# Optimization experiments

Measured on AMD Instinct MI355X. Metric: run time of the kernel, lower is better.

Reference implementation:

```python
import jax, jax.numpy as jnp
import numpy as np

B, LT, D, H, DI = 8, 128, 512, 8, 2048
NMEM, LMEM = 1024, 64
DH = D // H
EPS = 1e-5
NEG = -1e9

def _ln(x, g, b):
    mu = x.mean(-1, keepdims=True)
    var = ((x - mu) ** 2).mean(-1, keepdims=True)
    return (x - mu) * jax.lax.rsqrt(var + EPS) * g + b

def _ffn(x, W1, b1, W2, b2):
    # PositionwiseFF with residual=True (dropout=0 / eval)
    return x + jax.nn.relu(x @ W1 + b1) @ W2 + b2

def setup_inputs():
    key = jax.random.key(0)
    ks = jax.random.split(key, 16)
    w = lambda i, shape: jax.random.normal(ks[i], shape, jnp.float32) * 0.02
    return {
        "dec_output": jax.random.normal(ks[0], (B, LT, D), jnp.float32),
        "mem_attn_out": jax.random.normal(ks[1], (B, LT, NMEM + 1), jnp.float32),
        "enc_out_mem": jax.random.normal(ks[2], (NMEM, LMEM, D), jnp.float32),
        "tgt_emb_mem": jax.random.normal(ks[3], (NMEM, LMEM, D), jnp.float32),
        "tgt_mask_mem": jax.random.randint(ks[4], (NMEM, LMEM), 0, 2, jnp.int32),
        "tgt_mask": jax.random.randint(ks[5], (B, LT), 0, 2, jnp.int32),
        "g0": jnp.ones((D,), jnp.float32), "be0": jnp.zeros((D,), jnp.float32),
        "g1": jnp.ones((D,), jnp.float32), "be1": jnp.zeros((D,), jnp.float32),
        "Wq": w(6, (D, D)), "bq": jnp.zeros((D,), jnp.float32),
        "Wk": w(7, (D, D)), "bk": jnp.zeros((D,), jnp.float32),
        "Wv": w(8, (D, D)), "bv": jnp.zeros((D,), jnp.float32),
        "Wo": w(9, (D, D)), "bo": jnp.zeros((D,), jnp.float32),
        "f1W1": w(10, (D, DI)), "f1b1": jnp.zeros((DI,), jnp.float32),
        "f1W2": w(11, (DI, D)), "f1b2": jnp.zeros((D,), jnp.float32),
        "f2W1": w(12, (D, DI)), "f2b1": jnp.zeros((DI,), jnp.float32),
        "f2W2": w(13, (DI, D)), "f2b2": jnp.zeros((D,), jnp.float32),
    }

def reference(dec_output, mem_attn_out, enc_out_mem, tgt_emb_mem, tgt_mask_mem, tgt_mask,
              g0, be0, g1, be1, Wq, bq, Wk, bk, Wv, bv, Wo, bo,
              f1W1, f1b1, f1W2, f1b2, f2W1, f2b1, f2W2, f2b2):
    x = _ln(dec_output, g0, be0)                       # [B,LT,D]
    N = B * LT
    samples = jnp.argmax(mem_attn_out, -1).reshape(N) - 1   # [-1, NMEM-1]
    valid = samples >= 0                               # [N]
    s = jnp.maximum(samples, 0)                        # clamp; masked later
    q = x.reshape(N, 1, D)
    # gather memory per selected query (torch compacts via unique; same math)
    k_in = enc_out_mem[s]                              # [N,LMEM,D]
    v_in = tgt_emb_mem[s]                              # [N,LMEM,D]
    kmask = tgt_mask_mem[s] != 0                       # True = valid key
    # multi-head attention, residual=True
    qh = (q @ Wq + bq).reshape(N, 1, H, DH).transpose(0, 2, 1, 3)     # [N,H,1,DH]
    kh = (k_in @ Wk + bk).reshape(N, LMEM, H, DH).transpose(0, 2, 1, 3)
    vh = (v_in @ Wv + bv).reshape(N, LMEM, H, DH).transpose(0, 2, 1, 3)
    scores = jnp.einsum('nhqd,nhkd->nhqk', qh, kh) / (DH ** 0.5)      # [N,H,1,LMEM]
    scores = jnp.where(kmask[:, None, None, :], scores, NEG)
    attn = jax.nn.softmax(scores, axis=-1)
    ctx = jnp.einsum('nhqk,nhkd->nhqd', attn, vh).transpose(0, 2, 1, 3).reshape(N, 1, D)
    st = q + ctx @ Wo + bo
    st = _ffn(st, f1W1, f1b1, f1W2, f1b2)
    st = _ln(st, g1, be1)
    # scatter back: positions with sample == -1 get zeros
    st = jnp.where(valid[:, None, None], st, 0.0)
    dec = x + st.reshape(B, LT, D)
    dec = _ffn(dec, f2W1, f2b1, f2W2, f2b2)
    return dec
```

## Files before the change

### kernel.cpp

```cpp
#include <hip/hip_runtime.h>
#include <math.h>

#define NQ   1024
#define DIM  512
#define NH   8
#define DHD  64
#define DFF  2048
#define LM   64

typedef __bf16 bf16x8 __attribute__((ext_vector_type(8)));
typedef float  f32x4  __attribute__((ext_vector_type(4)));

__device__ __forceinline__ unsigned short f2bf(float f) {
    unsigned u = __builtin_bit_cast(unsigned, f);
    return (unsigned short)((u + 0x7fffu + ((u >> 16) & 1u)) >> 16);
}
__device__ __forceinline__ float bflo(unsigned p) {
    return __builtin_bit_cast(float, p << 16);
}
__device__ __forceinline__ float bfhi(unsigned p) {
    return __builtin_bit_cast(float, p & 0xffff0000u);
}

__device__ __forceinline__ void gload16(const void* g, void* l) {
    __builtin_amdgcn_global_load_lds(
        (const __attribute__((address_space(1))) unsigned*)g,
        (__attribute__((address_space(3))) unsigned*)l, 16, 0, 0);
}

__device__ __forceinline__ float blk_sum(float v, volatile float* red) {
#pragma unroll
    for (int o = 32; o; o >>= 1) v += __shfl_down(v, o);
    __syncthreads();
    if ((threadIdx.x & 63) == 0) red[threadIdx.x >> 6] = v;
    __syncthreads();
    return red[0] + red[1] + red[2] + red[3];
}

struct PrepPtrs {
    const float* src[8];
    unsigned short* dst[8];
};
__global__ __launch_bounds__(256) void prep_ln0_k(
    PrepPtrs p,
    const float* __restrict__ dec_out, const float* __restrict__ attn_out,
    const float* __restrict__ g, const float* __restrict__ be,
    float* __restrict__ x, unsigned* __restrict__ xb, int* __restrict__ samples)
{
    __shared__ float tile[32][33];
    __shared__ float red[4];
    __shared__ float rv[4]; __shared__ int ri[4];
    const int bid = blockIdx.x;

    if (bid < 5120) {
        int m, lt;
        if (bid < 1024) { m = bid >> 8; lt = bid & 255; }
        else { m = 4 + ((bid - 1024) >> 10); lt = (bid - 1024) & 1023; }
        const int RS = (m < 4) ? 512 : ((m == 5 || m == 7) ? 2048 : 512);
        const int CS = (m < 4) ? 512 : ((m == 5 || m == 7) ? 512 : 2048);
        const int TC = CS >> 5;
        const int tr = lt / TC, tc = lt % TC;
        const float* s = p.src[m];
        unsigned short* d = p.dst[m];
        const int tx = threadIdx.x & 31, ty = threadIdx.x >> 5;
        if (m == 1) {
#pragma unroll
            for (int i = 0; i < 32; i += 8) {
                size_t idx = (size_t)(tr * 32 + ty + i) * CS + tc * 32 + tx;
                d[idx] = f2bf(s[idx]);
            }
        } else {
#pragma unroll
            for (int i = 0; i < 32; i += 8)
                tile[ty + i][tx] = s[(size_t)(tr * 32 + ty + i) * CS + tc * 32 + tx];
            __syncthreads();
#pragma unroll
            for (int i = 0; i < 32; i += 8)
                d[(size_t)(tc * 32 + ty + i) * RS + tr * 32 + tx] = f2bf(tile[tx][ty + i]);
        }
        return;
    }

    const int n = bid - 5120, t = threadIdx.x;
    float2 v = ((const float2*)(dec_out + (size_t)n * DIM))[t];
    float mu  = blk_sum(v.x + v.y, red) * (1.f / DIM);
    float dx = v.x - mu, dy = v.y - mu;
    float var = blk_sum(dx * dx + dy * dy, red) * (1.f / DIM);
    float rs = rsqrtf(var + 1e-5f);
    float2 gg = ((const float2*)g)[t], bb = ((const float2*)be)[t];
    float ox = dx * rs * gg.x + bb.x, oy = dy * rs * gg.y + bb.y;
    ((float2*)(x + (size_t)n * DIM))[t] = make_float2(ox, oy);
    xb[(size_t)n * 256 + t] = (unsigned)f2bf(ox) | ((unsigned)f2bf(oy) << 16);

    const float* ar = attn_out + (size_t)n * 1025;
    float bv = -INFINITY; int bi = 0x7fffffff;
    for (int i = t; i < 1025; i += 256) {
        float val = ar[i];
        if (val > bv || (val == bv && i < bi)) { bv = val; bi = i; }
    }
#pragma unroll
    for (int o = 32; o; o >>= 1) {
        float ov = __shfl_down(bv, o); int oi = __shfl_down(bi, o);
        if (ov > bv || (ov == bv && oi < bi)) { bv = ov; bi = oi; }
    }
    if ((t & 63) == 0) { rv[t >> 6] = bv; ri[t >> 6] = bi; }
    __syncthreads();
    if (t == 0) {
#pragma unroll
        for (int w = 1; w < 4; ++w)
            if (rv[w] > bv || (rv[w] == bv && ri[w] < bi)) { bv = rv[w]; bi = ri[w]; }
        samples[n] = bi - 1;
    }
}

template<bool RELU, bool BIAS, bool RES, bool WF32, bool WBF>
__global__ __launch_bounds__(256) void mfma_gemm(
    const unsigned short* __restrict__ A, const unsigned short* __restrict__ Bt,
    float* __restrict__ Cf, unsigned short* __restrict__ Cb,
    const float* __restrict__ bias, const float* __restrict__ res,
    int K, int lda, int ldb, int ldc,
    int sA, int sB, int sC, int sBias)
{
    __shared__ unsigned short Ab[2][64 * 64];
    __shared__ unsigned short Bb[2][64 * 64];
    const int t = threadIdx.x, lane = t & 63, wid = t >> 6;
    const int nx = gridDim.x;
    const int fid = blockIdx.y * nx + blockIdx.x;
    const int cpx = (nx * gridDim.y) >> 3;
    const int f2 = (fid & 7) * cpx + (fid >> 3);
    const int bn = (f2 % nx) * 64, bm = (f2 / nx) * 64, bz = blockIdx.z;
    const unsigned short* Abase = A + (size_t)bz * sA + (size_t)bm * lda;
    const unsigned short* Bbase = Bt + (size_t)bz * sB + (size_t)bn * ldb;

    const int r0 = wid * 16 + (lane >> 3);
    const int cbs = lane & 7;

#define STAGE_T(buf, base, ld, kt)                                              \
    {                                                                           \
        int r_ = r0;                                                            \
        gload16(base + (size_t)r_ * ld + (kt) * 64 + ((cbs ^ (r_ & 7)) << 3),   \
                &buf[(wid * 2 + 0) * 512]);                                     \
        r_ = r0 + 8;                                                            \
        gload16(base + (size_t)r_ * ld + (kt) * 64 + ((cbs ^ (r_ & 7)) << 3),   \
                &buf[(wid * 2 + 1) * 512]);                                     \
    }

    const int lr = lane & 15, lg = lane >> 4;
    const int wr = (wid >> 1) * 32, wc = (wid & 1) * 32;
    const int mA0 = wr + lr, mA1 = wr + 16 + lr;
    const int nB0 = wc + lr, nB1 = wc + 16 + lr;
    f32x4 acc[2][2] = {};

#define COMPUTE(b)                                                              \
    _Pragma("unroll")                                                           \
    for (int kk = 0; kk < 2; ++kk) {                                            \
        const int kb = kk * 4 + lg;                                             \
        bf16x8 a0 = *(const bf16x8*)&Ab[b][mA0 * 64 + ((kb ^ (mA0 & 7)) << 3)]; \
        bf16x8 a1 = *(const bf16x8*)&Ab[b][mA1 * 64 + ((kb ^ (mA1 & 7)) << 3)]; \
        bf16x8 b0 = *(const bf16x8*)&Bb[b][nB0 * 64 + ((kb ^ (nB0 & 7)) << 3)]; \
        bf16x8 b1 = *(const bf16x8*)&Bb[b][nB1 * 64 + ((kb ^ (nB1 & 7)) << 3)]; \
        acc[0][0] = __builtin_amdgcn_mfma_f32_16x16x32_bf16(a0, b0, acc[0][0], 0, 0, 0); \
        acc[0][1] = __builtin_amdgcn_mfma_f32_16x16x32_bf16(a0, b1, acc[0][1], 0, 0, 0); \
        acc[1][0] = __builtin_amdgcn_mfma_f32_16x16x32_bf16(a1, b0, acc[1][0], 0, 0, 0); \
        acc[1][1] = __builtin_amdgcn_mfma_f32_16x16x32_bf16(a1, b1, acc[1][1], 0, 0, 0); \
    }

    STAGE_T(Ab[0], Abase, lda, 0);
    STAGE_T(Bb[0], Bbase, ldb, 0);
    __syncthreads();
    const int NT = K >> 6;
    int cur = 0;
    for (int kt = 0; kt < NT; ++kt) {
        if (kt + 1 < NT) {
            STAGE_T(Ab[cur ^ 1], Abase, lda, kt + 1);
            STAGE_T(Bb[cur ^ 1], Bbase, ldb, kt + 1);
        }
        if (cur == 0) { COMPUTE(0); } else { COMPUTE(1); }
        __syncthreads();
        cur ^= 1;
    }

#pragma unroll
    for (int fm = 0; fm < 2; ++fm)
#pragma unroll
    for (int fn = 0; fn < 2; ++fn) {
        const int col = bn + wc + fn * 16 + lr;
        float bia = BIAS ? bias[bz * sBias + col] : 0.f;
#pragma unroll
        for (int r = 0; r < 4; ++r) {
            const int row = bm + wr + fm * 16 + lg * 4 + r;
            const size_t ci = (size_t)bz * sC + (size_t)row * ldc + col;
            float v = acc[fm][fn][r] + bia;
            if (RES) v += res[(size_t)row * ldc + col];
            if (RELU) v = fmaxf(v, 0.f);
            if (WF32) Cf[ci] = v;
            if (WBF)  Cb[ci] = f2bf(v);
        }
    }
#undef STAGE_T
#undef COMPUTE
}

__global__ __launch_bounds__(256) void attn_scores_k(
    const unsigned short* __restrict__ u_bf, const float* __restrict__ enc,
    const int* __restrict__ maskmem, const int* __restrict__ samples,
    unsigned short* __restrict__ p_half, float* __restrict__ msc)
{
    __shared__ float S_lds[2][32][8];
    const int n = blockIdx.x, kq = blockIdx.y, t = threadIdx.x;
    const int lane = t & 63, w = t >> 6;
    int s = samples[n]; if (s < 0) s = 0;

    const int keyloc = (w & 1) * 16 + (lane & 15);
    const int key = kq * 32 + keyloc;
    const int dh = w >> 1;
    const int lg = lane >> 4;
    const int h = lane & 15;
    const float4* kb = (const float4*)(enc + (size_t)s * (LM * DIM));
    const int base = key * 128 + dh * 64 + lg * 2;
    float4 pf[4][2];
#pragma unroll
    for (int ss = 0; ss < 4; ++ss) {
        pf[ss][0] = kb[base + ss * 8];
        pf[ss][1] = kb[base + ss * 8 + 1];
    }
    const unsigned short* ub = u_bf + (size_t)n * 4096 + (size_t)(h & 7) * 512 + dh * 256;
    f32x4 acc = {};
#pragma unroll
    for (int step = 0; step < 8; ++step) {
        float4 a0 = pf[step & 3][0], a1 = pf[step & 3][1];
        if (step + 4 < 8) {
            pf[step & 3][0] = kb[base + (step + 4) * 8];
            pf[step & 3][1] = kb[base + (step + 4) * 8 + 1];
        }
        bf16x8 af;
        af[0] = (__bf16)a0.x; af[1] = (__bf16)a0.y;
        af[2] = (__bf16)a0.z; af[3] = (__bf16)a0.w;
        af[4] = (__bf16)a1.x; af[5] = (__bf16)a1.y;
        af[6] = (__bf16)a1.z; af[7] = (__bf16)a1.w;
        bf16x8 bfr = *(const bf16x8*)&ub[(step * 4 + lg) * 8];
        acc = __builtin_amdgcn_mfma_f32_16x16x32_bf16(af, bfr, acc, 0, 0, 0);
    }
    if (h < 8) {
#pragma unroll
        for (int r = 0; r < 4; ++r)
            S_lds[dh][(w & 1) * 16 + lg * 4 + r][h] = acc[r];
    }
    __syncthreads();

    const int h2 = t >> 5, k2 = t & 31;
    float sc = (S_lds[0][k2][h2] + S_lds[1][k2][h2]) * 0.125f;
    const int mk = maskmem[(size_t)s * LM + kq * 32 + k2];
    sc = (mk != 0) ? sc : -1e9f;
    float m = sc;
#pragma unroll
    for (int o = 16; o; o >>= 1) m = fmaxf(m, __shfl_xor(m, o));
    float e = __expf(sc - m);
    float su = e;
#pragma unroll
    for (int o = 16; o; o >>= 1) su += __shfl_xor(su, o);
    p_half[((size_t)n * 2 + kq) * 256 + k2 * 8 + h2] = f2bf(e);
    if (k2 == 0)
        ((float2*)(msc + ((size_t)n * 2 + kq) * 16))[h2] = make_float2(m, su);
}

__global__ __launch_bounds__(256) void attn_pv_k(
    const unsigned short* __restrict__ p_half, const float* __restrict__ msc,
    const float* __restrict__ vemb, const int* __restrict__ samples,
    unsigned* __restrict__ a_bf)
{
    __shared__ uint4 P_lds[64];
    __shared__ float2 Red[3][8][64];
    __shared__ float Wh[2][8];
    const int dq = blockIdx.x, n = blockIdx.y, t = threadIdx.x;
    int s = samples[n]; if (s < 0) s = 0;

    if (t < 8) {
        float2 ms0 = ((const float2*)(msc + (size_t)n * 32))[t];
        float2 ms1 = ((const float2*)(msc + (size_t)n * 32 + 16))[t];
        float m = fmaxf(ms0.x, ms1.x);
        float w0 = __expf(ms0.x - m), w1 = __expf(ms1.x - m);
        float inv = 1.f / (ms0.y * w0 + ms1.y * w1);
        Wh[0][t] = w0 * inv; Wh[1][t] = w1 * inv;
    }
    __syncthreads();
    {
        const int k = t >> 2, hp = t & 3, kq = k >> 5;
        unsigned v = ((const unsigned*)p_half)[((size_t)n * 2 + kq) * 128 + (k & 31) * 4 + hp];
        float a = bflo(v) * Wh[kq][hp * 2];
        float b = bfhi(v) * Wh[kq][hp * 2 + 1];
        ((unsigned*)P_lds)[k * 4 + hp] = (unsigned)f2bf(a) | ((unsigned)f2bf(b) << 16);
    }
    __syncthreads();

    const int c = t & 63, kh = t >> 6;
    const float2* vb = (const float2*)(vemb + (size_t)s * (LM * DIM)) + dq * 64 + c;
    float2 acc8[8];
#pragma unroll
    for (int hh = 0; hh < 8; ++hh) acc8[hh] = make_float2(0.f, 0.f);
#pragma unroll 8
    for (int i = 0; i < 16; ++i) {
        const int k = kh * 16 + i;
        float2 v = vb[(size_t)k * 256];
        uint4 pr = P_lds[k];
        float p0 = bflo(pr.x), p1 = bfhi(pr.x);
        float p2 = bflo(pr.y), p3 = bfhi(pr.y);
        float p4 = bflo(pr.z), p5 = bfhi(pr.z);
        float p6 = bflo(pr.w), p7 = bfhi(pr.w);
        acc8[0].x = fmaf(p0, v.x, acc8[0].x); acc8[0].y = fmaf(p0, v.y, acc8[0].y);
        acc8[1].x = fmaf(p1, v.x, acc8[1].x); acc8[1].y = fmaf(p1, v.y, acc8[1].y);
        acc8[2].x = fmaf(p2, v.x, acc8[2].x); acc8[2].y = fmaf(p2, v.y, acc8[2].y);
        acc8[3].x = fmaf(p3, v.x, acc8[3].x); acc8[3].y = fmaf(p3, v.y, acc8[3].y);
        acc8[4].x = fmaf(p4, v.x, acc8[4].x); acc8[4].y = fmaf(p4, v.y, acc8[4].y);
        acc8[5].x = fmaf(p5, v.x, acc8[5].x); acc8[5].y = fmaf(p5, v.y, acc8[5].y);
        acc8[6].x = fmaf(p6, v.x, acc8[6].x); acc8[6].y = fmaf(p6, v.y, acc8[6].y);
        acc8[7].x = fmaf(p7, v.x, acc8[7].x); acc8[7].y = fmaf(p7, v.y, acc8[7].y);
    }
    if (kh > 0) {
#pragma unroll
        for (int hh = 0; hh < 8; ++hh) Red[kh - 1][hh][c] = acc8[hh];
    }
    __syncthreads();
    if (kh == 0) {
        unsigned* an = a_bf + (size_t)n * 2048 + dq * 64;
#pragma unroll
        for (int hh = 0; hh < 8; ++hh) {
            float2 r0 = Red[0][hh][c], r1 = Red[1][hh][c], r2 = Red[2][hh][c];
            float ox = acc8[hh].x + r0.x + r1.x + r2.x;
            float oy = acc8[hh].y + r0.y + r1.y + r2.y;
            an[hh * 256 + c] = (unsigned)f2bf(ox) | ((unsigned)f2bf(oy) << 16);
        }
    }
}

__global__ __launch_bounds__(256) void ln1_mask_add_k(
    const float* __restrict__ t1p, const float* __restrict__ st0,
    const float* __restrict__ b2, const float* __restrict__ g,
    const float* __restrict__ be, const int* __restrict__ samples,
    const float* __restrict__ x, float* __restrict__ dec, unsigned* __restrict__ decb)
{
    __shared__ float red[4];
    const int n = blockIdx.x, t = threadIdx.x;
    const size_t off = (size_t)n * DIM + t * 2;
    float2 p0 = *(const float2*)&t1p[off];
    float2 p1 = *(const float2*)&t1p[(size_t)NQ * DIM + off];
    float2 s0 = *(const float2*)&st0[off];
    float2 b2v = ((const float2*)b2)[t];
    float2 v = make_float2(p0.x + p1.x + s0.x + b2v.x, p0.y + p1.y + s0.y + b2v.y);
    float mu  = blk_sum(v.x + v.y, red) * (1.f / DIM);
    float dx = v.x - mu, dy = v.y - mu;
    float var = blk_sum(dx * dx + dy * dy, red) * (1.f / DIM);
    float rs = rsqrtf(var + 1e-5f);
    float2 gg = ((const float2*)g)[t], bb = ((const float2*)be)[t];
    float sx = dx * rs * gg.x + bb.x, sy = dy * rs * gg.y + bb.y;
    if (samples[n] < 0) { sx = 0.f; sy = 0.f; }
    float2 xx = *(const float2*)&x[off];
    float ox = xx.x + sx, oy = xx.y + sy;
    *(float2*)&dec[off] = make_float2(ox, oy);
    decb[(size_t)n * 256 + t] = (unsigned)f2bf(ox) | ((unsigned)f2bf(oy) << 16);
}

extern "C" void kernel_launch(void* const* d_in, const int* in_sizes, int n_in,
                              void* d_out, int out_size, void* d_ws, size_t ws_size,
                              hipStream_t stream)
{
    const float* dec_output = (const float*)d_in[0];
    const float* mem_attn   = (const float*)d_in[1];
    const float* enc_mem    = (const float*)d_in[2];
    const float* temb_mem   = (const float*)d_in[3];
    const int*   mask_mem   = (const int*)d_in[4];
    const float* g0  = (const float*)d_in[6];
    const float* be0 = (const float*)d_in[7];
    const float* g1  = (const float*)d_in[8];
    const float* be1 = (const float*)d_in[9];
    const float* Wq  = (const float*)d_in[10];
    const float* bq  = (const float*)d_in[11];
    const float* Wk  = (const float*)d_in[12];
    const float* Wv  = (const float*)d_in[14];
    const float* bv  = (const float*)d_in[15];
    const float* Wo  = (const float*)d_in[16];
    const float* bo  = (const float*)d_in[17];
    const float* f1W1 = (const float*)d_in[18];
    const float* f1b1 = (const float*)d_in[19];
    const float* f1W2 = (const float*)d_in[20];
    const float* f1b2 = (const float*)d_in[21];
    const float* f2W1 = (const float*)d_in[22];
    const float* f2b1 = (const float*)d_in[23];
    const float* f2W2 = (const float*)d_in[24];
    const float* f2b2 = (const float*)d_in[25];
    float* out = (float*)d_out;

    float* ws = (float*)d_ws;
    float*          x_f   = ws + 0;
    unsigned*       x_b   = (unsigned*)(ws + 524288);
    unsigned short* qh_b  = (unsigned short*)(ws + 786432);
    unsigned short* u_b   = (unsigned short*)(ws + 1048576);
    unsigned short* a_b   = (unsigned short*)(ws + 3145728);
    unsigned short* p_hlf = (unsigned short*)(ws + 5242880);
    float*          msc   = ws + 5505024;
    unsigned short* wqt   = (unsigned short*)(ws + 7340032);
    unsigned short* wkc   = (unsigned short*)(ws + 7471104);
    unsigned short* wvt   = (unsigned short*)(ws + 7602176);
    unsigned short* wot   = (unsigned short*)(ws + 7733248);
    unsigned short* f1w1t = (unsigned short*)(ws + 7864320);
    unsigned short* f1w2t = (unsigned short*)(ws + 8388608);
    unsigned short* f2w1t = (unsigned short*)(ws + 8912896);
    unsigned short* f2w2t = (unsigned short*)(ws + 9437184);
    int*            smp   = (int*)(ws + 9961472);
    float*          t1p_f = ws + 9962496;
    float*          st0_f = (float*)u_b + 0;
    unsigned short* st0_b = (unsigned short*)((float*)u_b + 524288);
    float*          dec_f = (float*)u_b + 655360;
    unsigned*       dec_b = (unsigned*)((float*)u_b + 1179648);
    unsigned short* h1_b  = a_b;
    unsigned short* h2_b  = (unsigned short*)((float*)a_b + 1048576);

    PrepPtrs pp;
    pp.src[0] = Wq;   pp.dst[0] = wqt;
    pp.src[1] = Wk;   pp.dst[1] = wkc;
    pp.src[2] = Wv;   pp.dst[2] = wvt;
    pp.src[3] = Wo;   pp.dst[3] = wot;
    pp.src[4] = f1W1; pp.dst[4] = f1w1t;
    pp.src[5] = f1W2; pp.dst[5] = f1w2t;
    pp.src[6] = f2W1; pp.dst[6] = f2w1t;
    pp.src[7] = f2W2; pp.dst[7] = f2w2t;
    prep_ln0_k<<<5120 + NQ, 256, 0, stream>>>(pp, dec_output, mem_attn, g0, be0,
                                              x_f, x_b, smp);
    mfma_gemm<false, true, false, false, true><<<dim3(8, 16, 1), 256, 0, stream>>>(
        (const unsigned short*)x_b, wqt, nullptr, qh_b, bq, nullptr,
        DIM, DIM, DIM, DIM, 0, 0, 0, 0);
    mfma_gemm<false, false, false, false, true><<<dim3(8, 16, NH), 256, 0, stream>>>(
        qh_b, wkc, nullptr, u_b, nullptr, nullptr,
        DHD, DIM, DIM, NH * DIM, DHD, DHD, DIM, 0);
    attn_scores_k<<<dim3(NQ, 2), 256, 0, stream>>>(u_b, enc_mem, mask_mem, smp,
                                                   p_hlf, msc);
    attn_pv_k<<<dim3(4, NQ), 256, 0, stream>>>(p_hlf, msc, temb_mem, smp,
                                               (unsigned*)a_b);
    mfma_gemm<false, true, false, false, true><<<dim3(1, 16, NH), 256, 0, stream>>>(
        a_b, wvt, nullptr, qh_b, bv, nullptr,
        DIM, NH * DIM, DIM, DIM, DIM, DHD * DIM, DHD, DHD);
    mfma_gemm<false, true, true, true, true><<<dim3(8, 16, 1), 256, 0, stream>>>(
        qh_b, wot, st0_f, st0_b, bo, x_f, DIM, DIM, DIM, DIM, 0, 0, 0, 0);
    mfma_gemm<true, true, false, false, true><<<dim3(32, 16, 1), 256, 0, stream>>>(
        st0_b, f1w1t, nullptr, h1_b, f1b1, nullptr, DIM, DIM, DIM, DFF, 0, 0, 0, 0);
    mfma_gemm<false, false, false, true, false><<<dim3(8, 16, 2), 256, 0, stream>>>(
        h1_b, f1w2t, t1p_f, nullptr, nullptr, nullptr,
        1024, DFF, DFF, DIM, 1024, 1024, NQ * DIM, 0);
    ln1_mask_add_k<<<NQ, 256, 0, stream>>>(t1p_f, st0_f, f1b2, g1, be1, smp,
                                           x_f, dec_f, dec_b);
    mfma_gemm<true, true, false, false, true><<<dim3(32, 16, 1), 256, 0, stream>>>(
        (const unsigned short*)dec_b, f2w1t, nullptr, h2_b, f2b1, nullptr,
        DIM, DIM, DIM, DFF, 0, 0, 0, 0);
    mfma_gemm<false, true, true, true, false><<<dim3(8, 16, 1), 256, 0, stream>>>(
        h2_b, f2w2t, out, nullptr, f2b2, dec_f, DFF, DFF, DFF, DIM, 0, 0, 0, 0);

    (void)in_sizes; (void)n_in; (void)out_size; (void)ws_size;
}
```

Baseline: 153.2 us.

## Group queries by selected memory slot to reuse gathered K/V across queries

Adds a single-block kernel that buckets the 1024 queries by their sampled memory index using counting and a prefix scan. The attention score and PV kernels then launch one block per memory slot, load that slot's keys or values into registers once, and loop over every query mapped to it. This removes repeated global reads of the same enc/tgt memory rows when several queries pick the same slot. In exchange it adds a serial build kernel, load imbalance across blocks, extra syncs inside the per-query loops, and blocks that exit early for unused slots.

```diff
diff --git a/kernel.cpp b/kernel.cpp
--- a/kernel.cpp
+++ b/kernel.cpp
@@ -7,6 +7,7 @@
 #define DHD  64
 #define DFF  2048
 #define LM   64
+#define NMEM 1024
 
 typedef __bf16 bf16x8 __attribute__((ext_vector_type(8)));
 typedef float  f32x4  __attribute__((ext_vector_type(4)));
@@ -113,6 +114,50 @@
     }
 }
 
+__global__ __launch_bounds__(1024) void group_build_k(
+    const int* __restrict__ samples, int* __restrict__ qcount,
+    int* __restrict__ qstart, int* __restrict__ qlist)
+{
+    __shared__ int cnt[NMEM];
+    __shared__ int base[NMEM];
+    __shared__ int wsum[16];
+    const int t = threadIdx.x;
+    cnt[t] = 0;
+    __syncthreads();
+    int s = samples[t]; if (s < 0) s = 0;
+    atomicAdd(&cnt[s], 1);
+    __syncthreads();
+    const int c = cnt[t];
+    int v = c;
+    const int lane = t & 63, w = t >> 6;
+#pragma unroll
+    for (int o = 1; o < 64; o <<= 1) {
+        int u = __shfl_up(v, o);
+        if (lane >= o) v += u;
+    }
+    if (lane == 63) wsum[w] = v;
+    __syncthreads();
+    if (w == 0) {
+        int x = (lane < 16) ? wsum[lane] : 0;
+#pragma unroll
+        for (int o = 1; o < 16; o <<= 1) {
+            int u = __shfl_up(x, o);
+            if (lane >= o) x += u;
+        }
+        if (lane < 16) wsum[lane] = x;
+    }
+    __syncthreads();
+    const int start = v - c + (w ? wsum[w - 1] : 0);
+    base[t] = start;
+    qstart[t] = start;
+    qcount[t] = c;
+    __syncthreads();
+    cnt[t] = 0;
+    __syncthreads();
+    int pos = atomicAdd(&cnt[s], 1);
+    qlist[base[s] + pos] = t;
+}
+
 template<bool RELU, bool BIAS, bool RES, bool WF32, bool WBF>
 __global__ __launch_bounds__(256) void mfma_gemm(
     const unsigned short* __restrict__ A, const unsigned short* __restrict__ Bt,
@@ -203,13 +248,17 @@
 
 __global__ __launch_bounds__(256) void attn_scores_k(
     const unsigned short* __restrict__ u_bf, const float* __restrict__ enc,
-    const int* __restrict__ maskmem, const int* __restrict__ samples,
+    const int* __restrict__ maskmem,
+    const int* __restrict__ qcount, const int* __restrict__ qstart,
+    const int* __restrict__ qlist,
     unsigned short* __restrict__ p_half, float* __restrict__ msc)
 {
     __shared__ float S_lds[2][32][8];
-    const int n = blockIdx.x, kq = blockIdx.y, t = threadIdx.x;
+    __shared__ int Msk_lds[32];
+    const int s = blockIdx.x, kq = blockIdx.y, t = threadIdx.x;
+    const int cnt = qcount[s];
+    if (cnt == 0) return;
     const int lane = t & 63, w = t >> 6;
-    int s = samples[n]; if (s < 0) s = 0;
 
     const int keyloc = (w & 1) * 16 + (lane & 15);
     const int key = kq * 32 + keyloc;
@@ -218,117 +267,135 @@
     const int h = lane & 15;
     const float4* kb = (const float4*)(enc + (size_t)s * (LM * DIM));
     const int base = key * 128 + dh * 64 + lg * 2;
-    float4 pf[4][2];
-#pragma unroll
-    for (int ss = 0; ss < 4; ++ss) {
-        pf[ss][0] = kb[base + ss * 8];
-        pf[ss][1] = kb[base + ss * 8 + 1];
-    }
-    const unsigned short* ub = u_bf + (size_t)n * 4096 + (size_t)(h & 7) * 512 + dh * 256;
-    f32x4 acc = {};
-#pragma unroll
-    for (int step = 0; step < 8; ++step) {
-        float4 a0 = pf[step & 3][0], a1 = pf[step & 3][1];
-        if (step + 4 < 8) {
-            pf[step & 3][0] = kb[base + (step + 4) * 8];
-            pf[step & 3][1] = kb[base + (step + 4) * 8 + 1];
-        }
-        bf16x8 af;
-        af[0] = (__bf16)a0.x; af[1] = (__bf16)a0.y;
-        af[2] = (__bf16)a0.z; af[3] = (__bf16)a0.w;
-        af[4] = (__bf16)a1.x; af[5] = (__bf16)a1.y;
-        af[6] = (__bf16)a1.z; af[7] = (__bf16)a1.w;
-        bf16x8 bfr = *(const bf16x8*)&ub[(step * 4 + lg) * 8];
-        acc = __builtin_amdgcn_mfma_f32_16x16x32_bf16(af, bfr, acc, 0, 0, 0);
-    }
-    if (h < 8) {
-#pragma unroll
-        for (int r = 0; r < 4; ++r)
-            S_lds[dh][(w & 1) * 16 + lg * 4 + r][h] = acc[r];
-    }
-    __syncthreads();
-
-    const int h2 = t >> 5, k2 = t & 31;
-    float sc = (S_lds[0][k2][h2] + S_lds[1][k2][h2]) * 0.125f;
-    const int mk = maskmem[(size_t)s * LM + kq * 32 + k2];
-    sc = (mk != 0) ? sc : -1e9f;
-    float m = sc;
-#pragma unroll
-    for (int o = 16; o; o >>= 1) m = fmaxf(m, __shfl_xor(m, o));
-    float e = __expf(sc - m);
-    float su = e;
-#pragma unroll
-    for (int o = 16; o; o >>= 1) su += __shfl_xor(su, o);
-    p_half[((size_t)n * 2 + kq) * 256 + k2 * 8 + h2] = f2bf(e);
-    if (k2 == 0)
-        ((float2*)(msc + ((size_t)n * 2 + kq) * 16))[h2] = make_float2(m, su);
+    bf16x8 afr[8];
+    {
+        float4 buf[8][2];
+#pragma unroll
+        for (int st = 0; st < 8; ++st) {
+            buf[st][0] = kb[base + st * 8];
+            buf[st][1] = kb[base + st * 8 + 1];
+        }
+#pragma unroll
+        for (int st = 0; st < 8; ++st) {
+            float4 a0 = buf[st][0], a1 = buf[st][1];
+            afr[st][0] = (__bf16)a0.x; afr[st][1] = (__bf16)a0.y;
+            afr[st][2] = (__bf16)a0.z; afr[st][3] = (__bf16)a0.w;
+            afr[st][4] = (__bf16)a1.x; afr[st][5] = (__bf16)a1.y;
+            afr[st][6] = (__bf16)a1.z; afr[st][7] = (__bf16)a1.w;
+        }
+    }
+    if (t < 32) Msk_lds[t] = maskmem[(size_t)s * LM + kq * 32 + t];
+
+    const int qs = qstart[s];
+    for (int g = 0; g < cnt; ++g) {
+        const int q = qlist[qs + g];
+        const unsigned short* ub =
+            u_bf + (size_t)q * 4096 + (size_t)(h & 7) * 512 + dh * 256;
+        f32x4 acc = {};
+#pragma unroll
+        for (int st = 0; st < 8; ++st) {
+            bf16x8 bfr = *(const bf16x8*)&ub[(st * 4 + lg) * 8];
+            acc = __builtin_amdgcn_mfma_f32_16x16x32_bf16(afr[st], bfr, acc, 0, 0, 0);
+        }
+        __syncthreads();
+        if (h < 8) {
+#pragma unroll
+            for (int r = 0; r < 4; ++r)
+                S_lds[dh][(w & 1) * 16 + lg * 4 + r][h] = acc[r];
+        }
+        __syncthreads();
+        const int h2 = t >> 5, k2 = t & 31;
+        float sc = (S_lds[0][k2][h2] + S_lds[1][k2][h2]) * 0.125f;
+        sc = (Msk_lds[k2] != 0) ? sc : -1e9f;
+        float m = sc;
+#pragma unroll
+        for (int o = 16; o; o >>= 1) m = fmaxf(m, __shfl_xor(m, o));
+        float e = __expf(sc - m);
+        float su = e;
+#pragma unroll
+        for (int o = 16; o; o >>= 1) su += __shfl_xor(su, o);
+        p_half[((size_t)q * 2 + kq) * 256 + k2 * 8 + h2] = f2bf(e);
+        if (k2 == 0)
+            ((float2*)(msc + ((size_t)q * 2 + kq) * 16))[h2] = make_float2(m, su);
+    }
 }
 
 __global__ __launch_bounds__(256) void attn_pv_k(
     const unsigned short* __restrict__ p_half, const float* __restrict__ msc,
-    const float* __restrict__ vemb, const int* __restrict__ samples,
-    unsigned* __restrict__ a_bf)
+    const float* __restrict__ vemb,
+    const int* __restrict__ qcount, const int* __restrict__ qstart,
+    const int* __restrict__ qlist, unsigned* __restrict__ a_bf)
 {
     __shared__ uint4 P_lds[64];
     __shared__ float2 Red[3][8][64];
     __shared__ float Wh[2][8];
-    const int dq = blockIdx.x, n = blockIdx.y, t = threadIdx.x;
-    int s = samples[n]; if (s < 0) s = 0;
-
-    if (t < 8) {
-        float2 ms0 = ((const float2*)(msc + (size_t)n * 32))[t];
-        float2 ms1 = ((const float2*)(msc + (size_t)n * 32 + 16))[t];
-        float m = fmaxf(ms0.x, ms1.x);
-        float w0 = __expf(ms0.x - m), w1 = __expf(ms1.x - m);
-        float inv = 1.f / (ms0.y * w0 + ms1.y * w1);
-        Wh[0][t] = w0 * inv; Wh[1][t] = w1 * inv;
-    }
-    __syncthreads();
-    {
-        const int k = t >> 2, hp = t & 3, kq = k >> 5;
-        unsigned v = ((const unsigned*)p_half)[((size_t)n * 2 + kq) * 128 + (k & 31) * 4 + hp];
-        float a = bflo(v) * Wh[kq][hp * 2];
-        float b = bfhi(v) * Wh[kq][hp * 2 + 1];
-        ((unsigned*)P_lds)[k * 4 + hp] = (unsigned)f2bf(a) | ((unsigned)f2bf(b) << 16);
-    }
-    __syncthreads();
+    const int s = blockIdx.x, dq = blockIdx.y, t = threadIdx.x;
+    const int cnt = qcount[s];
+    if (cnt == 0) return;
 
     const int c = t & 63, kh = t >> 6;
     const float2* vb = (const float2*)(vemb + (size_t)s * (LM * DIM)) + dq * 64 + c;
-    float2 acc8[8];
-#pragma unroll
-    for (int hh = 0; hh < 8; ++hh) acc8[hh] = make_float2(0.f, 0.f);
-#pragma unroll 8
-    for (int i = 0; i < 16; ++i) {
-        const int k = kh * 16 + i;
-        float2 v = vb[(size_t)k * 256];
-        uint4 pr = P_lds[k];
-        float p0 = bflo(pr.x), p1 = bfhi(pr.x);
-        float p2 = bflo(pr.y), p3 = bfhi(pr.y);
-        float p4 = bflo(pr.z), p5 = bfhi(pr.z);
-        float p6 = bflo(pr.w), p7 = bfhi(pr.w);
-        acc8[0].x = fmaf(p0, v.x, acc8[0].x); acc8[0].y = fmaf(p0, v.y, acc8[0].y);
-        acc8[1].x = fmaf(p1, v.x, acc8[1].x); acc8[1].y = fmaf(p1, v.y, acc8[1].y);
-        acc8[2].x = fmaf(p2, v.x, acc8[2].x); acc8[2].y = fmaf(p2, v.y, acc8[2].y);
-        acc8[3].x = fmaf(p3, v.x, acc8[3].x); acc8[3].y = fmaf(p3, v.y, acc8[3].y);
-        acc8[4].x = fmaf(p4, v.x, acc8[4].x); acc8[4].y = fmaf(p4, v.y, acc8[4].y);
-        acc8[5].x = fmaf(p5, v.x, acc8[5].x); acc8[5].y = fmaf(p5, v.y, acc8[5].y);
-        acc8[6].x = fmaf(p6, v.x, acc8[6].x); acc8[6].y = fmaf(p6, v.y, acc8[6].y);
-        acc8[7].x = fmaf(p7, v.x, acc8[7].x); acc8[7].y = fmaf(p7, v.y, acc8[7].y);
-    }
-    if (kh > 0) {
-#pragma unroll
-        for (int hh = 0; hh < 8; ++hh) Red[kh - 1][hh][c] = acc8[hh];
-    }
-    __syncthreads();
-    if (kh == 0) {
-        unsigned* an = a_bf + (size_t)n * 2048 + dq * 64;
-#pragma unroll
-        for (int hh = 0; hh < 8; ++hh) {
-            float2 r0 = Red[0][hh][c], r1 = Red[1][hh][c], r2 = Red[2][hh][c];
-            float ox = acc8[hh].x + r0.x + r1.x + r2.x;
-            float oy = acc8[hh].y + r0.y + r1.y + r2.y;
-            an[hh * 256 + c] = (unsigned)f2bf(ox) | ((unsigned)f2bf(oy) << 16);
+    float2 vreg[16];
+#pragma unroll
+    for (int i = 0; i < 16; ++i) vreg[i] = vb[(size_t)(kh * 16 + i) * 256];
+
+    const int qs = qstart[s];
+    for (int g = 0; g < cnt; ++g) {
+        const int q = qlist[qs + g];
+        __syncthreads();
+        if (t < 8) {
+            float2 ms0 = ((const float2*)(msc + (size_t)q * 32))[t];
+            float2 ms1 = ((const float2*)(msc + (size_t)q * 32 + 16))[t];
+            float m = fmaxf(ms0.x, ms1.x);
+            float w0 = __expf(ms0.x - m), w1 = __expf(ms1.x - m);
+            float inv = 1.f / (ms0.y * w0 + ms1.y * w1);
+            Wh[0][t] = w0 * inv; Wh[1][t] = w1 * inv;
+        }
+        __syncthreads();
+        {
+            const int k = t >> 2, hp = t & 3, kq2 = k >> 5;
+            unsigned v = ((const unsigned*)p_half)[((size_t)q * 2 + kq2) * 128 + (k & 31) * 4 + hp];
+            float a = bflo(v) * Wh[kq2][hp * 2];
+            float b = bfhi(v) * Wh[kq2][hp * 2 + 1];
+            ((unsigned*)P_lds)[k * 4 + hp] = (unsigned)f2bf(a) | ((unsigned)f2bf(b) << 16);
+        }
+        __syncthreads();
+
+        float2 acc8[8];
+#pragma unroll
+        for (int hh = 0; hh < 8; ++hh) acc8[hh] = make_float2(0.f, 0.f);
+#pragma unroll
+        for (int i = 0; i < 16; ++i) {
+            const int k = kh * 16 + i;
+            float2 v = vreg[i];
+            uint4 pr = P_lds[k];
+            float p0 = bflo(pr.x), p1 = bfhi(pr.x);
+            float p2 = bflo(pr.y), p3 = bfhi(pr.y);
+            float p4 = bflo(pr.z), p5 = bfhi(pr.z);
+            float p6 = bflo(pr.w), p7 = bfhi(pr.w);
+            acc8[0].x = fmaf(p0, v.x, acc8[0].x); acc8[0].y = fmaf(p0, v.y, acc8[0].y);
+            acc8[1].x = fmaf(p1, v.x, acc8[1].x); acc8[1].y = fmaf(p1, v.y, acc8[1].y);
+            acc8[2].x = fmaf(p2, v.x, acc8[2].x); acc8[2].y = fmaf(p2, v.y, acc8[2].y);
+            acc8[3].x = fmaf(p3, v.x, acc8[3].x); acc8[3].y = fmaf(p3, v.y, acc8[3].y);
+            acc8[4].x = fmaf(p4, v.x, acc8[4].x); acc8[4].y = fmaf(p4, v.y, acc8[4].y);
+            acc8[5].x = fmaf(p5, v.x, acc8[5].x); acc8[5].y = fmaf(p5, v.y, acc8[5].y);
+            acc8[6].x = fmaf(p6, v.x, acc8[6].x); acc8[6].y = fmaf(p6, v.y, acc8[6].y);
+            acc8[7].x = fmaf(p7, v.x, acc8[7].x); acc8[7].y = fmaf(p7, v.y, acc8[7].y);
+        }
+        if (kh > 0) {
+#pragma unroll
+            for (int hh = 0; hh < 8; ++hh) Red[kh - 1][hh][c] = acc8[hh];
+        }
+        __syncthreads();
+        if (kh == 0) {
+            unsigned* an = a_bf + (size_t)q * 2048 + dq * 64;
+#pragma unroll
+            for (int hh = 0; hh < 8; ++hh) {
+                float2 r0 = Red[0][hh][c], r1 = Red[1][hh][c], r2 = Red[2][hh][c];
+                float ox = acc8[hh].x + r0.x + r1.x + r2.x;
+                float oy = acc8[hh].y + r0.y + r1.y + r2.y;
+                an[hh * 256 + c] = (unsigned)f2bf(ox) | ((unsigned)f2bf(oy) << 16);
+            }
         }
     }
 }
@@ -407,7 +474,10 @@
     unsigned short* f2w1t = (unsigned short*)(ws + 8912896);
     unsigned short* f2w2t = (unsigned short*)(ws + 9437184);
     int*            smp   = (int*)(ws + 9961472);
-    float*          t1p_f = ws + 9962496;
+    int*            qcnt  = (int*)(ws + 9962496);
+    int*            qsta  = (int*)(ws + 9963520);
+    int*            qlst  = (int*)(ws + 9964544);
+    float*          t1p_f = ws + 9965568;
     float*          st0_f = (float*)u_b + 0;
     unsigned short* st0_b = (unsigned short*)((float*)u_b + 524288);
     float*          dec_f = (float*)u_b + 655360;
@@ -426,16 +496,17 @@
     pp.src[7] = f2W2; pp.dst[7] = f2w2t;
     prep_ln0_k<<<5120 + NQ, 256, 0, stream>>>(pp, dec_output, mem_attn, g0, be0,
                                               x_f, x_b, smp);
+    group_build_k<<<1, 1024, 0, stream>>>(smp, qcnt, qsta, qlst);
     mfma_gemm<false, true, false, false, true><<<dim3(8, 16, 1), 256, 0, stream>>>(
         (const unsigned short*)x_b, wqt, nullptr, qh_b, bq, nullptr,
         DIM, DIM, DIM, DIM, 0, 0, 0, 0);
     mfma_gemm<false, false, false, false, true><<<dim3(8, 16, NH), 256, 0, stream>>>(
         qh_b, wkc, nullptr, u_b, nullptr, nullptr,
         DHD, DIM, DIM, NH * DIM, DHD, DHD, DIM, 0);
-    attn_scores_k<<<dim3(NQ, 2), 256, 0, stream>>>(u_b, enc_mem, mask_mem, smp,
-                                                   p_hlf, msc);
-    attn_pv_k<<<dim3(4, NQ), 256, 0, stream>>>(p_hlf, msc, temb_mem, smp,
-                                               (unsigned*)a_b);
+    attn_scores_k<<<dim3(NMEM, 2), 256, 0, stream>>>(u_b, enc_mem, mask_mem,
+                                                     qcnt, qsta, qlst, p_hlf, msc);
+    attn_pv_k<<<dim3(NMEM, 4), 256, 0, stream>>>(p_hlf, msc, temb_mem,
+                                                 qcnt, qsta, qlst, (unsigned*)a_b);
     mfma_gemm<false, true, false, false, true><<<dim3(1, 16, NH), 256, 0, stream>>>(
         a_b, wvt, nullptr, qh_b, bv, nullptr,
         DIM, NH * DIM, DIM, DIM, DIM, DHD * DIM, DHD, DHD);
```

Measured after the change: 177.1 us. +15.6%, slower.
